# Kernel optimization log

Measured on AMD Instinct MI355X. Metric: run time of the kernel, lower is better.

Reference implementation:

```python
import math
import jax
import jax.numpy as jnp
import numpy as np

N_NODE = 50000
N_EDGE = 1_600_000
D_IN = 128
D_K = 32
N_HEADS = 8


def setup_inputs() -> dict:
    key = jax.random.key(0)
    k_h, k_e, k_q, k_k, k_v = jax.random.split(key, 5)
    h = jax.random.normal(k_h, (N_NODE, D_IN), dtype=jnp.float32)
    edge_idx = jax.random.randint(k_e, (2, N_EDGE), 0, N_NODE, dtype=jnp.int64)
    scale = 1.0 / math.sqrt(D_IN)
    WQ = jax.random.normal(k_q, (N_HEADS, D_IN, D_K), dtype=jnp.float32) * scale
    WK = jax.random.normal(k_k, (N_HEADS, D_IN, D_K), dtype=jnp.float32) * scale
    WV = jax.random.normal(k_v, (N_HEADS, D_IN, D_K), dtype=jnp.float32) * scale
    return {"h": h, "edge_idx": edge_idx, "WQ": WQ, "WK": WK, "WV": WV}


def reference(h, edge_idx, WQ, WK, WV):
    n_node = h.shape[0]
    d_k = WK.shape[-1]
    # Per-head projections: [H, N, d]
    Q = jnp.einsum('nd,hdk->hnk', h, WQ)
    K = jnp.einsum('nd,hdk->hnk', h, WK)
    V = jnp.einsum('nd,hdv->hnv', h, WV)
    row = edge_idx[0]  # destination (softmax normalized per row, dim=1)
    col = edge_idx[1]  # source
    # Edge logits: e[h, e] = <Q[h, row[e]], K[h, col[e]]> / sqrt(d_k)
    e = jnp.einsum('hek,hek->he', Q[:, row, :], K[:, col, :]) / jnp.sqrt(
        jnp.asarray(d_k, dtype=h.dtype))
    eT = e.T  # [E, H]
    # Sparse (segment) softmax over outgoing edges of each row node.
    m = jax.ops.segment_max(eT, row, num_segments=n_node)  # [N, H]
    m = jnp.where(jnp.isfinite(m), m, jnp.zeros_like(m))   # guard empty rows
    ex = jnp.exp(eT - m[row])                               # [E, H]
    denom = jax.ops.segment_sum(ex, row, num_segments=n_node)  # [N, H]
    att = ex / denom[row]                                   # [E, H]
    # Sparse mm: out[i] = sum_{edges (i,j)} att * V[j]
    msgs = att[:, :, None] * jnp.transpose(V, (1, 0, 2))[col]  # [E, H, d_v]
    out = jax.ops.segment_sum(msgs, row, num_segments=n_node)  # [N, H, d_v]
    # aggregate == 'concat' -> head-major concat along feature dim
    return out.reshape(n_node, -1)
```

## Files before the change

### kernel.cpp

```cpp
#include <hip/hip_runtime.h>
#include <hip/hip_bf16.h>
#include <cstdint>

#define D_IN 128
#define DK 32
#define NH 8
#define HD 256

typedef __attribute__((ext_vector_type(8))) short short8;
typedef __attribute__((ext_vector_type(4))) float f32x4;
typedef _Float16 h2v __attribute__((ext_vector_type(2)));

__device__ inline float u2f(unsigned int u) {
  union { unsigned int i; float f; } c; c.i = u; return c.f;
}
__device__ inline short f2bf(float f) {
  union { float f; unsigned int i; } c; c.f = f;
  unsigned int u = c.i;
  u = u + 0x7FFFu + ((u >> 16) & 1u);
  return (short)(u >> 16);
}
__device__ inline short f2h(float f) {
  union { _Float16 h; short s; } c; c.h = (_Float16)f; return c.s;
}
__device__ inline h2v u2h2(unsigned int u) {
  union { unsigned int u; h2v h; } c; c.u = u; return c.h;
}

__global__ __launch_bounds__(256) void prep_w_kernel(
    const float* __restrict__ WQ, const float* __restrict__ WK,
    const float* __restrict__ WV, short8* __restrict__ Bbuf) {
  int ct = blockIdx.x;
  int t = threadIdx.x;
  int kt = t >> 6, L = t & 63;
  int col = ct * 16 + (L & 15);
  int type = col >> 8;
  const float* W = (type == 0) ? WQ : (type == 1) ? WK : WV;
  int head = (col & 255) >> 5;
  int kk = col & 31;
  int k0 = kt * 32 + ((L >> 4) << 3);
  short8 o;
  #pragma unroll
  for (int r = 0; r < 8; r++)
    o[r] = f2bf(W[head * (D_IN * DK) + (k0 + r) * DK + kk]);
  Bbuf[(size_t)(ct * 4 + kt) * 64 + L] = o;
}

__global__ __launch_bounds__(256) void gemm_qkv_kernel(
    const float* __restrict__ h, const short8* __restrict__ Bbuf,
    short* __restrict__ Qh, short* __restrict__ KVh,
    int nt_total, int n_node) {
  __shared__ float hs[16][132];
  __shared__ short lds[16][768];
  int nt = blockIdx.x;
  int t = threadIdx.x;
  {
    const float4* h4 = (const float4*)(h + (size_t)nt * 16 * 128);
    float4 v0 = h4[t * 2], v1 = h4[t * 2 + 1];
    int node = t >> 4, dim = (t & 15) * 8;
    hs[node][dim + 0] = v0.x; hs[node][dim + 1] = v0.y;
    hs[node][dim + 2] = v0.z; hs[node][dim + 3] = v0.w;
    hs[node][dim + 4] = v1.x; hs[node][dim + 5] = v1.y;
    hs[node][dim + 6] = v1.z; hs[node][dim + 7] = v1.w;
  }
  __syncthreads();
  int w = t >> 6;
  int L = t & 63;
  int arow = L & 15, k0base = ((L >> 4) << 3);
  short8 afrag[4];
  #pragma unroll
  for (int kt = 0; kt < 4; kt++) {
    #pragma unroll
    for (int r = 0; r < 8; r++)
      afrag[kt][r] = f2bf(hs[arow][kt * 32 + k0base + r]);
  }
  f32x4 acc[12];
  #pragma unroll
  for (int c = 0; c < 12; c++) acc[c] = (f32x4){0.f, 0.f, 0.f, 0.f};
  #pragma unroll
  for (int kt = 0; kt < 4; kt++) {
    #pragma unroll
    for (int c = 0; c < 12; c++) {
      short8 b = Bbuf[(size_t)((w * 12 + c) * 4 + kt) * 64 + L];
      acc[c] = __builtin_amdgcn_mfma_f32_16x16x32_bf16(afrag[kt], b, acc[c], 0, 0, 0);
    }
  }
  int row0 = (L >> 4) << 2;
  int col0 = w * 192 + (L & 15);
  const float QSL = 0.25506966f;
  #pragma unroll
  for (int c = 0; c < 12; c++) {
    float sc = ((w * 192 + c * 16) < 256) ? QSL : 1.f;
    #pragma unroll
    for (int r = 0; r < 4; r++)
      lds[row0 + r][col0 + c * 16] = f2h(acc[c][r] * sc);
  }
  __syncthreads();
  #pragma unroll
  for (int j = 0; j < 2; j++) {
    int u = t + j * 256;
    int hh = u >> 6, r2 = (u >> 2) & 15, part = u & 3;
    float4 vdat = *(const float4*)&lds[r2][hh * 32 + part * 8];
    *(float4*)(Qh + ((size_t)hh * n_node + nt * 16 + r2) * 32 + part * 8) = vdat;
  }
  #pragma unroll
  for (int j = 0; j < 4; j++) {
    int u = t + j * 256;
    int hh = u >> 7, r2 = (u >> 3) & 15, part = u & 7;
    int srccol = (part < 4) ? (256 + hh * 32 + part * 8)
                            : (512 + hh * 32 + (part - 4) * 8);
    float4 vdat = *(const float4*)&lds[r2][srccol];
    *(float4*)(KVh + ((size_t)hh * n_node + nt * 16 + r2) * 64 +
               ((part < 4) ? part * 8 : 32 + (part - 4) * 8)) = vdat;
  }
}

__global__ void rank_kernel(const int* __restrict__ row, int n_edge,
                            int* __restrict__ cnt, int* __restrict__ rank) {
  int i = blockIdx.x * blockDim.x + threadIdx.x;
  if (i < n_edge) rank[i] = atomicAdd(&cnt[row[i]], 1);
}

__global__ __launch_bounds__(256) void scan1_kernel(
    const int* __restrict__ cnt, int n, int* __restrict__ exc,
    int* __restrict__ bsum) {
  __shared__ int s[256];
  int gid = blockIdx.x * 256 + threadIdx.x;
  int v = (gid < n) ? cnt[gid] : 0;
  s[threadIdx.x] = v;
  __syncthreads();
  #pragma unroll
  for (int off = 1; off < 256; off <<= 1) {
    int t = (threadIdx.x >= off) ? s[threadIdx.x - off] : 0;
    __syncthreads();
    s[threadIdx.x] += t;
    __syncthreads();
  }
  if (gid < n) exc[gid] = s[threadIdx.x] - v;
  if (threadIdx.x == 255) bsum[blockIdx.x] = s[255];
}

__global__ __launch_bounds__(256) void scan2_kernel(int* __restrict__ bsum,
                                                    int nb) {
  __shared__ int s[256];
  int v = (threadIdx.x < nb) ? bsum[threadIdx.x] : 0;
  s[threadIdx.x] = v;
  __syncthreads();
  #pragma unroll
  for (int off = 1; off < 256; off <<= 1) {
    int t = (threadIdx.x >= off) ? s[threadIdx.x - off] : 0;
    __syncthreads();
    s[threadIdx.x] += t;
    __syncthreads();
  }
  if (threadIdx.x < nb) bsum[threadIdx.x] = s[threadIdx.x] - v;
}

__global__ __launch_bounds__(256) void scan3_kernel(
    int* __restrict__ exc, const int* __restrict__ bsum, int n, int n_edge) {
  int gid = blockIdx.x * 256 + threadIdx.x;
  if (gid < n) exc[gid] = exc[gid] + bsum[blockIdx.x];
  if (gid == 0) exc[n] = n_edge;
}

__global__ void scatter_kernel(const int* __restrict__ row,
                               const int* __restrict__ col,
                               const int* __restrict__ rank, int n_edge,
                               const int* __restrict__ offsets,
                               int* __restrict__ col_sorted) {
  int i = blockIdx.x * blockDim.x + threadIdx.x;
  if (i < n_edge) col_sorted[offsets[row[i]] + rank[i]] = col[i];
}

#define PROC(r, vld)                                                         \
  {                                                                          \
    h2v k0 = u2h2(r.x), k1 = u2h2(r.y), k2 = u2h2(r.z), k3 = u2h2(r.w);      \
    float d = __builtin_amdgcn_fdot2(k3, q3, 0.f, false);                    \
    d = __builtin_amdgcn_fdot2(k2, q2, d, false);                            \
    d = __builtin_amdgcn_fdot2(k1, q1, d, false);                            \
    d = __builtin_amdgcn_fdot2(k0, q0, d, false);                            \
    d += DPPF(d, 0xB1);                        \
    d += DPPF(d, 0x4E);                        \
    float tt = __shfl_xor(d, 4);              \
    float lg = (s < 4) ? d : tt;                                             \
    float p = (vld) ? exp2f(lg) : 0.f;                                       \
    float x0 = (float)k0[0], x1 = (float)k0[1];                              \
    float x2 = (float)k1[0], x3 = (float)k1[1];                              \
    float x4 = (float)k2[0], x5 = (float)k2[1];                              \
    float x6 = (float)k3[0], x7 = (float)k3[1];                              \
    dn += p;                                                                 \
    a0 = fmaf(p, x0, a0); a1 = fmaf(p, x1, a1);                              \
    a2 = fmaf(p, x2, a2); a3 = fmaf(p, x3, a3);                              \
    a4 = fmaf(p, x4, a4); a5 = fmaf(p, x5, a5);                              \
    a6 = fmaf(p, x6, a6); a7 = fmaf(p, x7, a7);                              \
  }

#define DPPF(x, ctrl)                                                         \
  ({                                                                          \
    union { float f; int i; } _a, _r;                                         \
    _a.f = (x);                                                               \
    _r.i = __builtin_amdgcn_update_dpp(0, _a.i, (ctrl), 0xF, 0xF, true);      \
    _r.f;                                                                     \
  })

__global__ __launch_bounds__(256) void attn_kernel(
    const short* __restrict__ Qh, const short* __restrict__ KVh,
    const int* __restrict__ offsets, const int* __restrict__ col_sorted,
    float* __restrict__ out, int n_node) {
  int head = blockIdx.x & 7;
  int grp = blockIdx.x >> 3;
  int wv = threadIdx.x >> 6;
  int lane = threadIdx.x & 63;
  int g = lane >> 3;
  int s = lane & 7;
  int node = grp * 4 + wv;
  if (node >= n_node) return;
  int start = offsets[node], end = offsets[node + 1];

  if (end <= start) {
    if (g == 0 && s >= 4) {
      float* op = out + (size_t)node * HD + head * 32 + (s - 4) * 8;
      float4 z = make_float4(0.f, 0.f, 0.f, 0.f);
      *(float4*)op = z;
      *(float4*)(op + 4) = z;
    }
    return;
  }

  h2v q0, q1, q2, q3;
  {
    uint4 qr = *(const uint4*)((const char*)(Qh +
                ((size_t)head * n_node + node) * 32) + (s & 3) * 16);
    q0 = u2h2(qr.x); q1 = u2h2(qr.y); q2 = u2h2(qr.z); q3 = u2h2(qr.w);
  }
  float dn = 0.f;
  float a0 = 0.f, a1 = 0.f, a2 = 0.f, a3 = 0.f;
  float a4 = 0.f, a5 = 0.f, a6 = 0.f, a7 = 0.f;

  const char* kvb = (const char*)KVh + (size_t)head * n_node * 128;
  unsigned int soff = (unsigned int)s << 4;

  for (int base = start; base < end; base += 16) {
    int i0 = base + g, i1 = base + 8 + g;
    bool v0 = i0 < end, v1 = i1 < end;
    int c0 = col_sorted[v0 ? i0 : start];
    int c1 = col_sorted[v1 ? i1 : start];
    unsigned int b0 = ((unsigned int)c0 << 7) + soff;
    unsigned int b1 = ((unsigned int)c1 << 7) + soff;
    uint4 r0 = *(const uint4*)(kvb + b0);
    uint4 r1 = *(const uint4*)(kvb + b1);
    PROC(r0, v0);
    PROC(r1, v1);
  }

  dn += __shfl_xor(dn, 8); dn += __shfl_xor(dn, 16); dn += __shfl_xor(dn, 32);
  a0 += __shfl_xor(a0, 8); a0 += __shfl_xor(a0, 16); a0 += __shfl_xor(a0, 32);
  a1 += __shfl_xor(a1, 8); a1 += __shfl_xor(a1, 16); a1 += __shfl_xor(a1, 32);
  a2 += __shfl_xor(a2, 8); a2 += __shfl_xor(a2, 16); a2 += __shfl_xor(a2, 32);
  a3 += __shfl_xor(a3, 8); a3 += __shfl_xor(a3, 16); a3 += __shfl_xor(a3, 32);
  a4 += __shfl_xor(a4, 8); a4 += __shfl_xor(a4, 16); a4 += __shfl_xor(a4, 32);
  a5 += __shfl_xor(a5, 8); a5 += __shfl_xor(a5, 16); a5 += __shfl_xor(a5, 32);
  a6 += __shfl_xor(a6, 8); a6 += __shfl_xor(a6, 16); a6 += __shfl_xor(a6, 32);
  a7 += __shfl_xor(a7, 8); a7 += __shfl_xor(a7, 16); a7 += __shfl_xor(a7, 32);

  float inv = 1.f / dn;
  if (g == 0 && s >= 4) {
    float* op = out + (size_t)node * HD + head * 32 + (s - 4) * 8;
    float4 o0 = make_float4(a0 * inv, a1 * inv, a2 * inv, a3 * inv);
    float4 o1 = make_float4(a4 * inv, a5 * inv, a6 * inv, a7 * inv);
    *(float4*)op = o0;
    *(float4*)(op + 4) = o1;
  }
}

extern "C" void kernel_launch(void* const* d_in, const int* in_sizes, int n_in,
                              void* d_out, int out_size, void* d_ws,
                              size_t ws_size, hipStream_t stream) {
  const float* h = (const float*)d_in[0];
  const int* edge = (const int*)d_in[1];
  const float* WQ = (const float*)d_in[2];
  const float* WK = (const float*)d_in[3];
  const float* WV = (const float*)d_in[4];
  float* out = (float*)d_out;

  int n_node = in_sizes[0] / D_IN;
  int n_edge = in_sizes[1] / 2;
  const int* row = edge;
  const int* col = edge + n_edge;

  char* ws = (char*)d_ws;
  size_t off = 0;
  auto alloc = [&](size_t bytes) {
    void* p = ws + off;
    off += (bytes + 255) & ~(size_t)255;
    return p;
  };
  int nt_total = (n_node + 15) / 16;
  short* Qh = (short*)alloc((size_t)NH * n_node * 32 * 2);
  short* KVh = (short*)alloc((size_t)NH * n_node * 64 * 2);
  short8* Bbuf = (short8*)alloc((size_t)48 * 4 * 64 * 16);
  int* col_sorted = (int*)alloc((size_t)n_edge * 4);
  int* rank = (int*)alloc((size_t)n_edge * 4);
  int* cnt = (int*)alloc((size_t)n_node * 4);
  int* offsets = (int*)alloc((size_t)(n_node + 1) * 4);
  int* bsum = (int*)alloc(256 * 4);

  hipMemsetAsync(cnt, 0, (size_t)n_node * 4, stream);

  prep_w_kernel<<<48, 256, 0, stream>>>(WQ, WK, WV, Bbuf);
  gemm_qkv_kernel<<<nt_total, 256, 0, stream>>>(h, Bbuf, Qh, KVh, nt_total,
                                                n_node);

  int nb_e = (n_edge + 255) / 256;
  rank_kernel<<<nb_e, 256, 0, stream>>>(row, n_edge, cnt, rank);

  int nb = (n_node + 255) / 256;
  scan1_kernel<<<nb, 256, 0, stream>>>(cnt, n_node, offsets, bsum);
  scan2_kernel<<<1, 256, 0, stream>>>(bsum, nb);
  scan3_kernel<<<nb, 256, 0, stream>>>(offsets, bsum, n_node, n_edge);

  scatter_kernel<<<nb_e, 256, 0, stream>>>(row, col, rank, n_edge, offsets,
                                           col_sorted);

  attn_kernel<<<((n_node + 3) / 4) * 8, 256, 0, stream>>>(
      Qh, KVh, offsets, col_sorted, out, n_node);
}
```

Measured before the change: 345.8 us.

## Remap attention lanes so each 4-lane quad handles both K and V per edge

The lane mapping changes from 8 lanes per edge (4 reading K, 4 reading V, joined by a cross-lane shuffle) to 4 lanes per edge, with each lane loading both its K and V slices. Each wave now covers 32 edges per iteration instead of 16, and the per-edge shfl_xor that passed the logit from the K lanes to the V lanes is gone. In exchange each lane issues twice the gather loads per iteration, and the final reduction adds one more shuffle stage per accumulator. Load-level parallelism for low-degree nodes may shift.

```diff
diff --git a/kernel.cpp b/kernel.cpp
--- a/kernel.cpp
+++ b/kernel.cpp
@@ -26,6 +26,13 @@
 __device__ inline h2v u2h2(unsigned int u) {
   union { unsigned int u; h2v h; } c; c.u = u; return c.h;
 }
+#define DPPF(x, ctrl)                                                         \
+  ({                                                                          \
+    union { float f; int i; } _a, _r;                                         \
+    _a.f = (x);                                                               \
+    _r.i = __builtin_amdgcn_update_dpp(0, _a.i, (ctrl), 0xF, 0xF, true);      \
+    _r.f;                                                                     \
+  })
 
 __global__ __launch_bounds__(256) void prep_w_kernel(
     const float* __restrict__ WQ, const float* __restrict__ WK,
@@ -172,36 +179,23 @@
   if (i < n_edge) col_sorted[offsets[row[i]] + rank[i]] = col[i];
 }
 
-#define PROC(r, vld)                                                         \
+#define QPROC(rk, rv, vld)                                                   \
   {                                                                          \
-    h2v k0 = u2h2(r.x), k1 = u2h2(r.y), k2 = u2h2(r.z), k3 = u2h2(r.w);      \
+    h2v k0 = u2h2(rk.x), k1 = u2h2(rk.y), k2 = u2h2(rk.z), k3 = u2h2(rk.w);  \
     float d = __builtin_amdgcn_fdot2(k3, q3, 0.f, false);                    \
     d = __builtin_amdgcn_fdot2(k2, q2, d, false);                            \
     d = __builtin_amdgcn_fdot2(k1, q1, d, false);                            \
     d = __builtin_amdgcn_fdot2(k0, q0, d, false);                            \
     d += DPPF(d, 0xB1);                        \
     d += DPPF(d, 0x4E);                        \
-    float tt = __shfl_xor(d, 4);              \
-    float lg = (s < 4) ? d : tt;                                             \
-    float p = (vld) ? exp2f(lg) : 0.f;                                       \
-    float x0 = (float)k0[0], x1 = (float)k0[1];                              \
-    float x2 = (float)k1[0], x3 = (float)k1[1];                              \
-    float x4 = (float)k2[0], x5 = (float)k2[1];                              \
-    float x6 = (float)k3[0], x7 = (float)k3[1];                              \
+    float p = (vld) ? exp2f(d) : 0.f;                                        \
     dn += p;                                                                 \
-    a0 = fmaf(p, x0, a0); a1 = fmaf(p, x1, a1);                              \
-    a2 = fmaf(p, x2, a2); a3 = fmaf(p, x3, a3);                              \
-    a4 = fmaf(p, x4, a4); a5 = fmaf(p, x5, a5);                              \
-    a6 = fmaf(p, x6, a6); a7 = fmaf(p, x7, a7);                              \
-  }
-
-#define DPPF(x, ctrl)                                                         \
-  ({                                                                          \
-    union { float f; int i; } _a, _r;                                         \
-    _a.f = (x);                                                               \
-    _r.i = __builtin_amdgcn_update_dpp(0, _a.i, (ctrl), 0xF, 0xF, true);      \
-    _r.f;                                                                     \
-  })
+    h2v v0 = u2h2(rv.x), v1 = u2h2(rv.y), v2 = u2h2(rv.z), v3 = u2h2(rv.w);  \
+    a0 = fmaf(p, (float)v0[0], a0); a1 = fmaf(p, (float)v0[1], a1);          \
+    a2 = fmaf(p, (float)v1[0], a2); a3 = fmaf(p, (float)v1[1], a3);          \
+    a4 = fmaf(p, (float)v2[0], a4); a5 = fmaf(p, (float)v2[1], a5);          \
+    a6 = fmaf(p, (float)v3[0], a6); a7 = fmaf(p, (float)v3[1], a7);          \
+  }
 
 __global__ __launch_bounds__(256) void attn_kernel(
     const short* __restrict__ Qh, const short* __restrict__ KVh,
@@ -211,15 +205,15 @@
   int grp = blockIdx.x >> 3;
   int wv = threadIdx.x >> 6;
   int lane = threadIdx.x & 63;
-  int g = lane >> 3;
-  int s = lane & 7;
+  int eslot = lane >> 2;
+  int q4 = lane & 3;
   int node = grp * 4 + wv;
   if (node >= n_node) return;
   int start = offsets[node], end = offsets[node + 1];
 
   if (end <= start) {
-    if (g == 0 && s >= 4) {
-      float* op = out + (size_t)node * HD + head * 32 + (s - 4) * 8;
+    if (lane < 4) {
+      float* op = out + (size_t)node * HD + head * 32 + q4 * 8;
       float4 z = make_float4(0.f, 0.f, 0.f, 0.f);
       *(float4*)op = z;
       *(float4*)(op + 4) = z;
@@ -230,7 +224,7 @@
   h2v q0, q1, q2, q3;
   {
     uint4 qr = *(const uint4*)((const char*)(Qh +
-                ((size_t)head * n_node + node) * 32) + (s & 3) * 16);
+                ((size_t)head * n_node + node) * 32) + q4 * 16);
     q0 = u2h2(qr.x); q1 = u2h2(qr.y); q2 = u2h2(qr.z); q3 = u2h2(qr.w);
   }
   float dn = 0.f;
@@ -238,34 +232,33 @@
   float a4 = 0.f, a5 = 0.f, a6 = 0.f, a7 = 0.f;
 
   const char* kvb = (const char*)KVh + (size_t)head * n_node * 128;
-  unsigned int soff = (unsigned int)s << 4;
-
-  for (int base = start; base < end; base += 16) {
-    int i0 = base + g, i1 = base + 8 + g;
+  unsigned int qoff = (unsigned int)q4 << 4;
+
+  for (int base = start; base < end; base += 32) {
+    int i0 = base + eslot, i1 = base + 16 + eslot;
     bool v0 = i0 < end, v1 = i1 < end;
     int c0 = col_sorted[v0 ? i0 : start];
     int c1 = col_sorted[v1 ? i1 : start];
-    unsigned int b0 = ((unsigned int)c0 << 7) + soff;
-    unsigned int b1 = ((unsigned int)c1 << 7) + soff;
-    uint4 r0 = *(const uint4*)(kvb + b0);
-    uint4 r1 = *(const uint4*)(kvb + b1);
-    PROC(r0, v0);
-    PROC(r1, v1);
-  }
-
-  dn += __shfl_xor(dn, 8); dn += __shfl_xor(dn, 16); dn += __shfl_xor(dn, 32);
-  a0 += __shfl_xor(a0, 8); a0 += __shfl_xor(a0, 16); a0 += __shfl_xor(a0, 32);
-  a1 += __shfl_xor(a1, 8); a1 += __shfl_xor(a1, 16); a1 += __shfl_xor(a1, 32);
-  a2 += __shfl_xor(a2, 8); a2 += __shfl_xor(a2, 16); a2 += __shfl_xor(a2, 32);
-  a3 += __shfl_xor(a3, 8); a3 += __shfl_xor(a3, 16); a3 += __shfl_xor(a3, 32);
-  a4 += __shfl_xor(a4, 8); a4 += __shfl_xor(a4, 16); a4 += __shfl_xor(a4, 32);
-  a5 += __shfl_xor(a5, 8); a5 += __shfl_xor(a5, 16); a5 += __shfl_xor(a5, 32);
-  a6 += __shfl_xor(a6, 8); a6 += __shfl_xor(a6, 16); a6 += __shfl_xor(a6, 32);
-  a7 += __shfl_xor(a7, 8); a7 += __shfl_xor(a7, 16); a7 += __shfl_xor(a7, 32);
+    unsigned int b0 = ((unsigned int)c0 << 7) + qoff;
+    unsigned int b1 = ((unsigned int)c1 << 7) + qoff;
+    uint4 rk0 = *(const uint4*)(kvb + b0);
+    uint4 rv0 = *(const uint4*)(kvb + b0 + 64);
+    uint4 rk1 = *(const uint4*)(kvb + b1);
+    uint4 rv1 = *(const uint4*)(kvb + b1 + 64);
+    QPROC(rk0, rv0, v0);
+    QPROC(rk1, rv1, v1);
+  }
+
+  dn += __shfl_xor(dn, 4); dn += __shfl_xor(dn, 8);
+  dn += __shfl_xor(dn, 16); dn += __shfl_xor(dn, 32);
+#define MRG(x)                                                               \
+  x += __shfl_xor(x, 4); x += __shfl_xor(x, 8);                              \
+  x += __shfl_xor(x, 16); x += __shfl_xor(x, 32);
+  MRG(a0) MRG(a1) MRG(a2) MRG(a3) MRG(a4) MRG(a5) MRG(a6) MRG(a7)
 
   float inv = 1.f / dn;
-  if (g == 0 && s >= 4) {
-    float* op = out + (size_t)node * HD + head * 32 + (s - 4) * 8;
+  if (lane < 4) {
+    float* op = out + (size_t)node * HD + head * 32 + q4 * 8;
     float4 o0 = make_float4(a0 * inv, a1 * inv, a2 * inv, a3 * inv);
     float4 o1 = make_float4(a4 * inv, a5 * inv, a6 * inv, a7 * inv);
     *(float4*)op = o0;
```

New measurement: 316.2 us (median of 2 runs). 1.09x faster.
